# Optimization experiments

Measured on AMD Instinct MI355X. Metric: run time of the kernel, lower is better.

## Reference

```python
import jax, jax.numpy as jnp
import numpy as np

NUM_EMBEDDINGS = 1024
EMBEDDING_DIM = 64
COMMITMENT_COST = 0.25


def setup_inputs() -> dict:
    key = jax.random.key(0)
    k1, k2 = jax.random.split(key)
    inputs = jax.random.normal(k1, (32, 64, 64, EMBEDDING_DIM), dtype=jnp.float32)
    # nn.Embedding init: uniform(-1/K, 1/K)
    weight = jax.random.uniform(k2, (NUM_EMBEDDINGS, EMBEDDING_DIM), dtype=jnp.float32,
                                minval=-1.0 / NUM_EMBEDDINGS, maxval=1.0 / NUM_EMBEDDINGS)
    return {"inputs": inputs, "weight": weight}


def reference(inputs, weight):
    K, D = weight.shape
    flat = inputs.reshape(-1, D)  # [N, D]
    distances = (jnp.sum(flat * flat, axis=1, keepdims=True)
                 + jnp.sum(weight * weight, axis=1)
                 - 2.0 * flat @ weight.T)
    encoding_indices = jnp.argmin(distances, axis=1)  # [N]
    # direct gather (math-equivalent to one-hot @ weight)
    quantized = weight[encoding_indices].reshape(inputs.shape)

    e_latent_loss = jnp.mean((jax.lax.stop_gradient(quantized) - inputs) ** 2)
    q_latent_loss = jnp.mean((quantized - jax.lax.stop_gradient(inputs)) ** 2)
    vq_loss = q_latent_loss + COMMITMENT_COST * e_latent_loss

    # avg_probs = mean over tokens of one-hot encodings == normalized histogram
    counts = jnp.zeros((K,), dtype=flat.dtype).at[encoding_indices].add(1.0)
    avg_probs = counts / flat.shape[0]
    perplexity = jnp.exp(-jnp.sum(avg_probs * jnp.log(avg_probs + 1e-10)))

    # straight-through estimator
    quantized_st = inputs + jax.lax.stop_gradient(quantized - inputs)
    return quantized_st, vq_loss, encoding_indices, perplexity
```

## Files before the change

kernel.cpp:

```cpp
#include <hip/hip_runtime.h>
#include <math.h>

#define N_TOK 131072
#define D     64
#define K     1024

#define OUT_LOSS  8388608
#define OUT_IDX   8388609
#define OUT_PERP  8519681


#define W_WINDOW 1e-4f

typedef short bf16x8 __attribute__((ext_vector_type(8)));
typedef float f32x4  __attribute__((ext_vector_type(4)));
typedef float vf16   __attribute__((ext_vector_type(16)));

#define SWZ(p) ((p) ^ ((((p) >> 7) & 7) << 4))

__device__ __forceinline__ float np_pairsum64(const float* sq) {
    float r[8];
#pragma unroll
    for (int j = 0; j < 8; ++j) r[j] = sq[j];
#pragma unroll
    for (int i = 8; i < 64; i += 8) {
#pragma unroll
        for (int j = 0; j < 8; ++j) r[j] = __fadd_rn(r[j], sq[i + j]);
    }
    return __fadd_rn(
        __fadd_rn(__fadd_rn(r[0], r[1]), __fadd_rn(r[2], r[3])),
        __fadd_rn(__fadd_rn(r[4], r[5]), __fadd_rn(r[6], r[7])));
}

__device__ __forceinline__ short bf16_trunc(float f) {
    return (short)(__float_as_uint(f) >> 16);
}
__device__ __forceinline__ float bf16_up(short s) {
    return __uint_as_float(((unsigned)(unsigned short)s) << 16);
}

__global__ void vq_prep(const float* __restrict__ w,
                        float* __restrict__ enorm,
                        float* __restrict__ sinit,
                        short* __restrict__ w_hi,
                        short* __restrict__ w_lo,
                        unsigned* __restrict__ counts,
                        float* __restrict__ sse,
                        unsigned* __restrict__ rcnt) {
    int k = blockIdx.x * blockDim.x + threadIdx.x;
    if (k < K) {
        const float* wr = w + (size_t)k * D;
        float sq[D];
        double acc = 0.0;
#pragma unroll
        for (int i = 0; i < D; ++i) {
            float v = wr[i];
            sq[i] = __fmul_rn(v, v);
            acc += (double)v * (double)v;
            short hi = bf16_trunc(v);
            float res = v - bf16_up(hi);
            short lo = bf16_trunc(res);
            w_hi[(size_t)k * D + i] = hi;
            w_lo[(size_t)k * D + i] = lo;
        }
        enorm[k] = np_pairsum64(sq);
        sinit[k] = (float)acc;
        counts[k] = 0u;
    }
    if (k == 0) { *sse = 0.f; *rcnt = 0u; }
}

#define MFMA(A, B, C) __builtin_amdgcn_mfma_f32_16x16x32_bf16(A, B, C, 0, 0, 0)

__device__ __forceinline__ void tile_step(
    int code, const bf16x8 (&Ah)[2][2], const bf16x8 (&Al)[2][2],
    bf16x8 H0, bf16x8 H1, bf16x8 L0, bf16x8 L1, float si,
    float (&m1)[8], float (&m2)[8], int (&i1)[8]) {
    f32x4 C0 = {si, si, si, si};
    f32x4 C1 = {si, si, si, si};
    C0 = MFMA(Ah[0][0], H0, C0); C0 = MFMA(Ah[0][1], H1, C0);
    C0 = MFMA(Ah[0][0], L0, C0); C0 = MFMA(Ah[0][1], L1, C0);
    C0 = MFMA(Al[0][0], H0, C0); C0 = MFMA(Al[0][1], H1, C0);
    C1 = MFMA(Ah[1][0], H0, C1); C1 = MFMA(Ah[1][1], H1, C1);
    C1 = MFMA(Ah[1][0], L0, C1); C1 = MFMA(Ah[1][1], L1, C1);
    C1 = MFMA(Al[1][0], H0, C1); C1 = MFMA(Al[1][1], H1, C1);
#pragma unroll
    for (int r = 0; r < 4; ++r) {
        {
            float c = C0[r];
            m2[r] = __builtin_amdgcn_fmed3f(m1[r], m2[r], c);
            bool lt = c < m1[r];
            i1[r] = lt ? code : i1[r];
            m1[r] = fminf(m1[r], c);
        }
        {
            float c = C1[r];
            m2[4 + r] = __builtin_amdgcn_fmed3f(m1[4 + r], m2[4 + r], c);
            bool lt = c < m1[4 + r];
            i1[4 + r] = lt ? code : i1[4 + r];
            m1[4 + r] = fminf(m1[4 + r], c);
        }
    }
}

__global__ __launch_bounds__(256, 4)
void vq_screen(const float* __restrict__ x,
               const float* __restrict__ sinit,
               const short* __restrict__ w_hi,
               const short* __restrict__ w_lo,
               const float* __restrict__ w,
               float* __restrict__ out,
               unsigned* __restrict__ counts,
               float* __restrict__ sse,
               int* __restrict__ rlist,
               unsigned* __restrict__ rcnt) {
    const int tid  = threadIdx.x;
    const int lane = tid & 63;
    const int wv   = __builtin_amdgcn_readfirstlane(tid >> 6);
    const int quad = lane >> 4;
    const int col  = lane & 15;
    const int tokWave = blockIdx.x * 128 + wv * 32;

    __shared__ short sB[2][2][4096];
    __shared__ float sS[1024];
    __shared__ int   smw[128];

    bf16x8 Ah[2][2], Al[2][2];
#pragma unroll
    for (int mt = 0; mt < 2; ++mt) {
#pragma unroll
        for (int ks = 0; ks < 2; ++ks) {
            const float4* ap = (const float4*)(x + (size_t)(tokWave + mt * 16 + col) * D
                                               + ks * 32 + quad * 8);
            float4 u0 = ap[0], u1 = ap[1];
            float f[8] = {u0.x, u0.y, u0.z, u0.w, u1.x, u1.y, u1.z, u1.w};
            bf16x8 h, l;
#pragma unroll
            for (int j = 0; j < 8; ++j) {
                float v = -2.0f * f[j];
                short hi = bf16_trunc(v);
                float res = v - bf16_up(hi);
                h[j] = hi;
                l[j] = bf16_trunc(res);
            }
            Ah[mt][ks] = h;
            Al[mt][ks] = l;
        }
    }

    float m1[8], m2[8];
    int   i1[8];
#pragma unroll
    for (int s = 0; s < 8; ++s) { m1[s] = INFINITY; m2[s] = INFINITY; i1[s] = 0; }

    const int  p0 = tid * 16;
    const int  p1 = p0 + 4096;
    const char* gh = (const char*)w_hi;
    const char* gl = (const char*)w_lo;

    {
        float4 g0 = *(const float4*)(gh + p0);
        float4 g1 = *(const float4*)(gh + p1);
        float4 g2 = *(const float4*)(gl + p0);
        float4 g3 = *(const float4*)(gl + p1);
        float4 s4 = *(const float4*)(sinit + tid * 4);
        char* lh = (char*)&sB[0][0][0];
        char* ll = (char*)&sB[0][1][0];
        *(float4*)(lh + SWZ(p0)) = g0;
        *(float4*)(lh + SWZ(p1)) = g1;
        *(float4*)(ll + SWZ(p0)) = g2;
        *(float4*)(ll + SWZ(p1)) = g3;
        *(float4*)(&sS[tid * 4]) = s4;
    }
    __syncthreads();

    for (int c = 0; c < 16; ++c) {
        const int buf = c & 1;
        const bool pf = (c < 15);
        float4 g0, g1, g2, g3;
        if (pf) {
            const size_t cb = (size_t)(c + 1) * 8192;
            g0 = *(const float4*)(gh + cb + p0);
            g1 = *(const float4*)(gh + cb + p1);
            g2 = *(const float4*)(gl + cb + p0);
            g3 = *(const float4*)(gl + cb + p1);
        }

        const char* lh = (const char*)&sB[buf][0][0];
        const char* ll = (const char*)&sB[buf][1][0];
#pragma unroll
        for (int tl = 0; tl < 4; ++tl) {
            const int r_ = tl * 16 + col;
            const int b0 = r_ * 128 + quad * 16;
            const int b1 = b0 + 64;
            bf16x8 H0 = *(const bf16x8*)(lh + SWZ(b0));
            bf16x8 H1 = *(const bf16x8*)(lh + SWZ(b1));
            bf16x8 L0 = *(const bf16x8*)(ll + SWZ(b0));
            bf16x8 L1 = *(const bf16x8*)(ll + SWZ(b1));
            const int tile = c * 4 + tl;
            const float si = sS[tile * 16 + col];
            tile_step(tile * 16 + col, Ah, Al, H0, H1, L0, L1, si, m1, m2, i1);
        }

        if (pf) {
            char* dh = (char*)&sB[buf ^ 1][0][0];
            char* dl = (char*)&sB[buf ^ 1][1][0];
            *(float4*)(dh + SWZ(p0)) = g0;
            *(float4*)(dh + SWZ(p1)) = g1;
            *(float4*)(dl + SWZ(p0)) = g2;
            *(float4*)(dl + SWZ(p1)) = g3;
        }
        __syncthreads();
    }

#pragma unroll
    for (int s = 0; s < 8; ++s) {
#pragma unroll
        for (int msk = 1; msk <= 8; msk <<= 1) {
            float om1 = __shfl_xor(m1[s], msk, 64);
            int   oi1 = __shfl_xor(i1[s], msk, 64);
            float om2 = __shfl_xor(m2[s], msk, 64);
            float nm2 = fminf(fmaxf(m1[s], om1), fminf(m2[s], om2));
            bool  take = om1 < m1[s];
            m1[s] = take ? om1 : m1[s];
            i1[s] = take ? oi1 : i1[s];
            m2[s] = nm2;
        }
    }

    if (col == 0) {
#pragma unroll
        for (int s = 0; s < 8; ++s) {
            int tl = (s >> 2) * 16 + quad * 4 + (s & 3);
            int tok = tokWave + tl;
            bool resc = (m2[s] <= m1[s] + W_WINDOW);
            if (resc) {
                unsigned u = atomicAdd(rcnt, 1u);
                rlist[u] = tok;
                smw[wv * 32 + tl] = -1;
            } else {
                atomicAdd(&counts[i1[s]], 1u);
                out[OUT_IDX + tok] = (float)i1[s];
                smw[wv * 32 + tl] = i1[s];
            }
        }
    }
    __syncthreads();

    const int sub = lane >> 4;
    const int fi  = lane & 15;
    float err = 0.f;
#pragma unroll
    for (int p = 0; p < 8; ++p) {
        const int tl  = wv * 32 + p * 4 + sub;
        const int tok = blockIdx.x * 128 + tl;
        const int wi2 = smw[tl];
        if (wi2 >= 0) {
            float4 q  = ((const float4*)(w + (size_t)wi2 * D))[fi];
            float4 xv = ((const float4*)(x + (size_t)tok * D))[fi];
            float e0 = q.x - xv.x, e1 = q.y - xv.y;
            float e2 = q.z - xv.z, e3 = q.w - xv.w;
            err = fmaf(e0, e0, err);
            err = fmaf(e1, e1, err);
            err = fmaf(e2, e2, err);
            err = fmaf(e3, e3, err);
            ((float4*)(out + (size_t)tok * D))[fi] = q;
        }
    }
#pragma unroll
    for (int o = 32; o > 0; o >>= 1) err += __shfl_down(err, o, 64);
    if (lane == 0) atomicAdd(sse, err);
}
#undef MFMA

#define XR(d) ((d) < 16 ? xa[(d) & 15] : (d) < 32 ? xb[(d) & 15] \
              : (d) < 48 ? xc[(d) & 15] : xd[(d) & 15])

__global__ __launch_bounds__(512, 2)
void vq_rescue(const float* __restrict__ x,
               const float* __restrict__ w,
               const float* __restrict__ enorm,
               float* __restrict__ out,
               unsigned* __restrict__ counts,
               float* __restrict__ sse,
               const int* __restrict__ rlist,
               const unsigned* __restrict__ rcnt) {
    const int lane = threadIdx.x & 63;
    const int wv   = __builtin_amdgcn_readfirstlane(threadIdx.x >> 6);
    const unsigned n = *rcnt;

    __shared__ float sd[8][64];
    __shared__ int   si[8][64];

    for (unsigned g = blockIdx.x; g * 64u < n; g += 256u) {
        const unsigned slot = g * 64u + (unsigned)lane;
        const bool valid = slot < n;
        const int t = valid ? rlist[slot] : 0;

        const vf16* xp = (const vf16*)(x + (size_t)t * D);
        vf16 xa = xp[0], xb = xp[1], xc = xp[2], xd = xp[3];

        float Sx;
        {
            float r0, r1, r2, r3, r4, r5, r6, r7;
#define SQ(n) __fmul_rn(XR(n), XR(n))
            r0 = SQ(0); r1 = SQ(1); r2 = SQ(2); r3 = SQ(3);
            r4 = SQ(4); r5 = SQ(5); r6 = SQ(6); r7 = SQ(7);
#define ACC8(i)                                                           \
            r0 = __fadd_rn(r0, SQ(8*(i)+0)); r1 = __fadd_rn(r1, SQ(8*(i)+1)); \
            r2 = __fadd_rn(r2, SQ(8*(i)+2)); r3 = __fadd_rn(r3, SQ(8*(i)+3)); \
            r4 = __fadd_rn(r4, SQ(8*(i)+4)); r5 = __fadd_rn(r5, SQ(8*(i)+5)); \
            r6 = __fadd_rn(r6, SQ(8*(i)+6)); r7 = __fadd_rn(r7, SQ(8*(i)+7));
            ACC8(1) ACC8(2) ACC8(3) ACC8(4) ACC8(5) ACC8(6) ACC8(7)
            Sx = __fadd_rn(
                __fadd_rn(__fadd_rn(r0, r1), __fadd_rn(r2, r3)),
                __fadd_rn(__fadd_rn(r4, r5), __fadd_rn(r6, r7)));
#undef ACC8
#undef SQ
        }

        float best = INFINITY;
        int   bidx = 0x7fffffff;
        const int c0 = wv * 128;
        for (int cc = 0; cc < 128; ++cc) {
            const int c = c0 + cc;
            const float* __restrict__ wr = w + (size_t)c * D;
            float a = 0.f;
#pragma unroll
            for (int d = 0; d < D; ++d) a = __fmaf_rn(wr[d], XR(d), a);
            float dist = __fsub_rn(__fadd_rn(Sx, enorm[c]), __fmul_rn(2.0f, a));
            bool lt = dist < best;
            best = lt ? dist : best;
            bidx = lt ? c : bidx;
        }
        sd[wv][lane] = best;
        si[wv][lane] = bidx;
        __syncthreads();

        if (wv == 0) {
            float b  = sd[0][lane];
            int   bi = si[0][lane];
#pragma unroll
            for (int j = 1; j < 8; ++j) {
                float dj = sd[j][lane];
                bool  l  = dj < b;
                b  = l ? dj : b;
                bi = l ? si[j][lane] : bi;
            }

            float err = 0.f;
            if (valid) {
                const float4* qr = (const float4*)(w + (size_t)bi * D);
                float4*       oq = (float4*)(out + (size_t)t * D);
#pragma unroll
                for (int i = 0; i < 16; ++i) {
                    float4 q = qr[i];
                    float e0 = q.x - XR(4 * i + 0);
                    float e1 = q.y - XR(4 * i + 1);
                    float e2 = q.z - XR(4 * i + 2);
                    float e3 = q.w - XR(4 * i + 3);
                    err = fmaf(e0, e0, err);
                    err = fmaf(e1, e1, err);
                    err = fmaf(e2, e2, err);
                    err = fmaf(e3, e3, err);
                    oq[i] = q;
                }
                out[OUT_IDX + t] = (float)bi;
                atomicAdd(&counts[bi], 1u);
            }
#pragma unroll
            for (int o = 32; o > 0; o >>= 1) err += __shfl_down(err, o, 64);
            if (lane == 0) atomicAdd(sse, err);
        }
        __syncthreads();
    }
}
#undef XR

__global__ void vq_fin(const unsigned* __restrict__ counts,
                       const float* __restrict__ sse,
                       float* __restrict__ out) {
    __shared__ float red[256];
    float s = 0.f;
    for (int k = threadIdx.x; k < K; k += 256) {
        float p = (float)counts[k] * (1.0f / (float)N_TOK);
        s += p * logf(p + 1e-10f);
    }
    red[threadIdx.x] = s;
    __syncthreads();
    for (int st = 128; st > 0; st >>= 1) {
        if (threadIdx.x < st) red[threadIdx.x] += red[threadIdx.x + st];
        __syncthreads();
    }
    if (threadIdx.x == 0) {
        out[OUT_PERP] = expf(-red[0]);
        out[OUT_LOSS] = 1.25f * (*sse) * (1.0f / 8388608.0f);
    }
}

extern "C" void kernel_launch(void* const* d_in, const int* in_sizes, int n_in,
                              void* d_out, int out_size, void* d_ws, size_t ws_size,
                              hipStream_t stream) {
    const float* x = (const float*)d_in[0];
    const float* w = (const float*)d_in[1];
    float* out = (float*)d_out;

    char* ws = (char*)d_ws;
    unsigned* counts = (unsigned*)(ws + 0);
    float*    enorm  = (float*)(ws + 4096);
    float*    sinit  = (float*)(ws + 8192);
    float*    sse    = (float*)(ws + 12288);
    unsigned* rcnt   = (unsigned*)(ws + 12292);
    short*    w_hi   = (short*)(ws + 16384);
    short*    w_lo   = (short*)(ws + 147456);
    int*      rlist  = (int*)(ws + 802816);

    vq_prep<<<4, 256, 0, stream>>>(w, enorm, sinit, w_hi, w_lo, counts, sse, rcnt);
    vq_screen<<<N_TOK / 128, 256, 0, stream>>>(x, sinit, w_hi, w_lo, w, out,
                                               counts, sse, rlist, rcnt);
    vq_rescue<<<256, 512, 0, stream>>>(x, w, enorm, out, counts, sse, rlist, rcnt);
    vq_fin<<<1, 256, 0, stream>>>(counts, sse, out);
}
```

Baseline: 267.9 us.

## Split screen epilogue into separate gather/loss kernel via winner index buffer

Moves the per-token epilogue (histogram atomics, index write, rescue-list append, quantized gather and SSE accumulation) out of the MFMA screening kernel into a new lightweight kernel. The screen kernel now only writes a winner index per token, with the high bit flagging tokens that need rescue. This is meant to keep the compute-bound screen kernel lean and free of the block-wide barrier and memory-bound tail, so it can run at higher occupancy. The cost is an extra launch and an extra round trip of the index buffer plus re-reading x.

```diff
diff --git a/kernel.cpp b/kernel.cpp
--- a/kernel.cpp
+++ b/kernel.cpp
@@ -108,12 +108,7 @@
                const float* __restrict__ sinit,
                const short* __restrict__ w_hi,
                const short* __restrict__ w_lo,
-               const float* __restrict__ w,
-               float* __restrict__ out,
-               unsigned* __restrict__ counts,
-               float* __restrict__ sse,
-               int* __restrict__ rlist,
-               unsigned* __restrict__ rcnt) {
+               int* __restrict__ win) {
     const int tid  = threadIdx.x;
     const int lane = tid & 63;
     const int wv   = __builtin_amdgcn_readfirstlane(tid >> 6);
@@ -123,7 +118,6 @@
 
     __shared__ short sB[2][2][4096];
     __shared__ float sS[1024];
-    __shared__ int   smw[128];
 
     bf16x8 Ah[2][2], Al[2][2];
 #pragma unroll
@@ -232,29 +226,49 @@
 #pragma unroll
         for (int s = 0; s < 8; ++s) {
             int tl = (s >> 2) * 16 + quad * 4 + (s & 3);
-            int tok = tokWave + tl;
             bool resc = (m2[s] <= m1[s] + W_WINDOW);
-            if (resc) {
-                unsigned u = atomicAdd(rcnt, 1u);
-                rlist[u] = tok;
-                smw[wv * 32 + tl] = -1;
-            } else {
-                atomicAdd(&counts[i1[s]], 1u);
-                out[OUT_IDX + tok] = (float)i1[s];
-                smw[wv * 32 + tl] = i1[s];
-            }
-        }
-    }
-    __syncthreads();
+            win[tokWave + tl] = resc ? (i1[s] | 0x80000000) : i1[s];
+        }
+    }
+}
+#undef MFMA
+
+__global__ __launch_bounds__(256, 8)
+void vq_epi(const float* __restrict__ x,
+            const float* __restrict__ w,
+            const int* __restrict__ win,
+            float* __restrict__ out,
+            unsigned* __restrict__ counts,
+            float* __restrict__ sse,
+            int* __restrict__ rlist,
+            unsigned* __restrict__ rcnt) {
+    const int lane = threadIdx.x & 63;
+    const int wv   = threadIdx.x >> 6;
+    const int tokBase = blockIdx.x * 64 + wv * 16;
+
+    int wiA = -1;
+    if (lane < 16) {
+        const int tok = tokBase + lane;
+        const int wi = win[tok];
+        if (wi < 0) {
+            unsigned u = atomicAdd(rcnt, 1u);
+            rlist[u] = tok;
+            wiA = -1;
+        } else {
+            atomicAdd(&counts[wi], 1u);
+            out[OUT_IDX + tok] = (float)wi;
+            wiA = wi;
+        }
+    }
 
     const int sub = lane >> 4;
     const int fi  = lane & 15;
     float err = 0.f;
 #pragma unroll
-    for (int p = 0; p < 8; ++p) {
-        const int tl  = wv * 32 + p * 4 + sub;
-        const int tok = blockIdx.x * 128 + tl;
-        const int wi2 = smw[tl];
+    for (int p = 0; p < 4; ++p) {
+        const int tl  = p * 4 + sub;
+        const int tok = tokBase + tl;
+        const int wi2 = __shfl(wiA, tl, 64);
         if (wi2 >= 0) {
             float4 q  = ((const float4*)(w + (size_t)wi2 * D))[fi];
             float4 xv = ((const float4*)(x + (size_t)tok * D))[fi];
@@ -271,7 +285,6 @@
     for (int o = 32; o > 0; o >>= 1) err += __shfl_down(err, o, 64);
     if (lane == 0) atomicAdd(sse, err);
 }
-#undef MFMA
 
 #define XR(d) ((d) < 16 ? xa[(d) & 15] : (d) < 32 ? xb[(d) & 15] \
               : (d) < 48 ? xc[(d) & 15] : xd[(d) & 15])
@@ -413,11 +426,12 @@
     unsigned* rcnt   = (unsigned*)(ws + 12292);
     short*    w_hi   = (short*)(ws + 16384);
     short*    w_lo   = (short*)(ws + 147456);
+    int*      win    = (int*)(ws + 278528);
     int*      rlist  = (int*)(ws + 802816);
 
     vq_prep<<<4, 256, 0, stream>>>(w, enorm, sinit, w_hi, w_lo, counts, sse, rcnt);
-    vq_screen<<<N_TOK / 128, 256, 0, stream>>>(x, sinit, w_hi, w_lo, w, out,
-                                               counts, sse, rlist, rcnt);
+    vq_screen<<<N_TOK / 128, 256, 0, stream>>>(x, sinit, w_hi, w_lo, win);
+    vq_epi<<<N_TOK / 64, 256, 0, stream>>>(x, w, win, out, counts, sse, rlist, rcnt);
     vq_rescue<<<256, 512, 0, stream>>>(x, w, enorm, out, counts, sse, rlist, rcnt);
     vq_fin<<<1, 256, 0, stream>>>(counts, sse, out);
 }
```

New measurement: 342.8 us. +27.9%, slower.
